# Kernel optimization log

Hardware: AMD Instinct MI355X
Metric: run time of the kernel (lower is better)

Reference implementation:

```python
import jax, jax.numpy as jnp
import numpy as np

EPS = 1e-12  # matches torch.nn.functional.normalize eps

def _l2norm(x, axis=-1):
    n = jnp.sqrt(jnp.sum(x * x, axis=axis, keepdims=True))
    return x / jnp.maximum(n, EPS)

def setup_inputs() -> dict:
    key = jax.random.key(0)
    k1, k2 = jax.random.split(key)
    B, C, H, W = 16, 256, 32, 32
    K = 8192
    z = jax.random.normal(k1, (B, C, H, W), dtype=jnp.float32)
    # torch init: uniform(-1/K, 1/K)
    emb_weight = jax.random.uniform(k2, (K, C), dtype=jnp.float32,
                                    minval=-1.0 / K, maxval=1.0 / K)
    return {"z": z, "emb_weight": emb_weight}

def reference(z, emb_weight):
    B, C, H, W = z.shape
    zt = jnp.transpose(z, (0, 2, 3, 1))            # [B,H,W,C]
    z_flat = zt.reshape(-1, C)                      # [N,C]
    zf_n = _l2norm(z_flat)                          # normalized tokens
    e_n = _l2norm(emb_weight)                       # normalized codebook [K,C]
    # squared euclidean distance via matmul (N x K)
    d = (jnp.sum(zf_n * zf_n, axis=1, keepdims=True)
         + jnp.sum(e_n * e_n, axis=1)
         - 2.0 * jnp.einsum('nc,kc->nk', zf_n, e_n))
    idx = jnp.argmin(d, axis=1)                     # [N]
    # get_codebook_entry: gather raw weight then normalize
    zq = _l2norm(emb_weight[idx])                   # [N,C]
    zq = zq.reshape(B, H, W, C)
    z_n = _l2norm(zt)                               # normalize z over channel dim
    # straight-through estimator
    zq = z_n + jax.lax.stop_gradient(zq - z_n)
    out = jnp.transpose(zq, (0, 3, 1, 2))           # [B,C,H,W]
    indices = idx.reshape(B, H, W)
    return out, indices
```

## Files before the change

### kernel.cpp

```cpp
#include <hip/hip_runtime.h>
#include <math.h>
#include <float.h>

#define K_CODES 8192
#define C_DIM   256
#define N_TOK   16384
#define B_      16
#define H_      32
#define W_      32
#define HW      1024
#define KSPLIT  16
#define TOKS_PER_BLK 256

typedef short  short8   __attribute__((ext_vector_type(8)));
typedef float  floatx16 __attribute__((ext_vector_type(16)));

__device__ inline ushort f32_to_bf16_rne(float x) {
    union { float f; unsigned u; } v; v.f = x;
    unsigned u = v.u;
    return (ushort)((u + 0x7FFFu + ((u >> 16) & 1u)) >> 16);
}
__device__ inline float bf16_bits_to_f32(ushort h) {
    union { unsigned u; float f; } v; v.u = ((unsigned)h) << 16;
    return v.f;
}
__device__ inline unsigned umax_(unsigned a, unsigned b) { return a > b ? a : b; }
__device__ inline unsigned umin_(unsigned a, unsigned b) { return a < b ? a : b; }

__device__ inline void g2l16(const void* g, void* l) {
    __builtin_amdgcn_global_load_lds((const __attribute__((address_space(1))) unsigned int*)g,
                                     (__attribute__((address_space(3))) unsigned int*)l,
                                     16, 0, 0);
}


__global__ __launch_bounds__(256) void norm_pack(
        const float* __restrict__ emb, const float* __restrict__ z,
        float* __restrict__ e_n, float* __restrict__ s2,
        ushort* __restrict__ Chi,
        float* __restrict__ ztn, ushort* __restrict__ Thi) {
    __shared__ float tile[32][257];
    __shared__ float pvt[32][9];
    __shared__ float pvt2[32][9];
    __shared__ float inv[32];
    int t = threadIdx.x;
    int bid = blockIdx.x;
    if (bid < 256) {
        int k0 = bid * 32;
        int r = t >> 3, cp = t & 7;
        const float* src = emb + (size_t)(k0 + r) * C_DIM + cp * 32;
        float ss = 0.f;
        #pragma unroll
        for (int j = 0; j < 8; ++j) {
            float4 v = *(const float4*)(src + j * 4);
            tile[r][cp * 32 + j * 4 + 0] = v.x;
            tile[r][cp * 32 + j * 4 + 1] = v.y;
            tile[r][cp * 32 + j * 4 + 2] = v.z;
            tile[r][cp * 32 + j * 4 + 3] = v.w;
            ss = fmaf(v.x, v.x, ss); ss = fmaf(v.y, v.y, ss);
            ss = fmaf(v.z, v.z, ss); ss = fmaf(v.w, v.w, ss);
        }
        pvt[r][cp] = ss;
        __syncthreads();
        if (t < 32) {
            float a = 0.f;
            #pragma unroll
            for (int p = 0; p < 8; ++p) a += pvt[t][p];
            inv[t] = 1.0f / fmaxf(sqrtf(a), 1e-12f);
        }
        __syncthreads();
        float iv = inv[r];
        float s2p = 0.f;
        float* dst = e_n + (size_t)(k0 + r) * C_DIM + cp * 32;
        #pragma unroll
        for (int j = 0; j < 8; ++j) {
            float a = tile[r][cp * 32 + j * 4 + 0] * iv;
            float b = tile[r][cp * 32 + j * 4 + 1] * iv;
            float c = tile[r][cp * 32 + j * 4 + 2] * iv;
            float d = tile[r][cp * 32 + j * 4 + 3] * iv;
            s2p = fmaf(a, a, s2p); s2p = fmaf(b, b, s2p);
            s2p = fmaf(c, c, s2p); s2p = fmaf(d, d, s2p);
            float4 o = {a, b, c, d};
            *(float4*)(dst + j * 4) = o;
        }
        pvt2[r][cp] = s2p;
        __syncthreads();
        if (t < 32) {
            float a = 0.f;
            #pragma unroll
            for (int p = 0; p < 8; ++p) a += pvt2[t][p];
            s2[k0 + t] = a;
        }
        char* chiB = (char*)Chi;
        #pragma unroll
        for (int e = 0; e < 4; ++e) {
            int p = e * 256 + t;
            int row = p & 31;
            int ch0 = ((p >> 6) << 4) | (((p >> 5) & 1) << 3);
            float rv = inv[row];
            union { ushort u[8]; uint4 v; } hs;
            #pragma unroll
            for (int i = 0; i < 8; ++i)
                hs.u[i] = f32_to_bf16_rne(tile[row][ch0 + i] * rv);
            size_t addr = (size_t)bid * 16384 + (size_t)p * 16;
            *(uint4*)(chiB + addr) = hs.v;
        }
    } else {
        int tb = bid - 256;
        int b = tb >> 5, h = tb & 31;
        int w = t & 31, c0 = t >> 5;
        const float* zb = z + ((size_t)(b * C_DIM) * H_ + h) * W_;
        #pragma unroll
        for (int it = 0; it < 32; ++it) {
            int c = it * 8 + c0;
            tile[w][c] = zb[(size_t)c * HW + w];
        }
        __syncthreads();
        int part = t >> 5, w2 = t & 31;
        float s = 0.f;
        #pragma unroll
        for (int i = 0; i < 32; ++i) {
            float v = tile[w2][part * 32 + i];
            s = fmaf(v, v, s);
        }
        pvt[w2][part] = s;
        __syncthreads();
        if (t < 32) {
            float ss = 0.f;
            #pragma unroll
            for (int p = 0; p < 8; ++p) ss += pvt[t][p];
            inv[t] = 1.0f / fmaxf(sqrtf(ss), 1e-12f);
        }
        __syncthreads();
        int n_base = tb * 32;
        for (int r = 0; r < 32; ++r) {
            float val = tile[r][t] * inv[r];
            ztn[(size_t)(n_base + r) * C_DIM + t] = val;
        }
        char* thiB = (char*)Thi;
        #pragma unroll
        for (int e = 0; e < 4; ++e) {
            int p = e * 256 + t;
            int row = p & 31;
            int ch0 = ((p >> 6) << 4) | (((p >> 5) & 1) << 3);
            float rv = inv[row];
            union { ushort u[8]; uint4 v; } hs;
            #pragma unroll
            for (int i = 0; i < 8; ++i)
                hs.u[i] = f32_to_bf16_rne(tile[row][ch0 + i] * rv);
            size_t addr = (size_t)tb * 16384 + (size_t)p * 16;
            *(uint4*)(thiB + addr) = hs.v;
        }
    }
}

__global__ __launch_bounds__(256, 2) void score_topk(
        const ushort* __restrict__ Chi,
        const ushort* __restrict__ Thi, uint2* __restrict__ cand) {
    __shared__ __align__(16) char smem[24576];
    int t = threadIdx.x;
    int l = t & 63, wv = t >> 6;
    int hh = l >> 5, col = l & 31;
    int tokBase = blockIdx.x * TOKS_PER_BLK;
    int tokRG = tokBase >> 5;
    int part = blockIdx.y;
    int partBase = part * (K_CODES / KSPLIT);
    int codeRGbase = partBase >> 5;

    const char* chiB = (const char*)Chi;
    const char* thiB = (const char*)Thi;

    unsigned rv1[2] = {0u, 0u}, rv2[2] = {0u, 0u}, rv3[2] = {0u, 0u};
    int ri1[2] = {0, 0}, ri2[2] = {0, 0}, ri3[2] = {0, 0};

    auto stage = [&](int skt, int ss, char* buf) {
        int codeRG = codeRGbase + skt * 4;
        #pragma unroll
        for (int gi = 0; gi < 3; ++gi) {
            int slice = wv * 3 + gi;
            const char* gb;
            int off;
            if (slice < 4) {
                gb = chiB + (size_t)(codeRG + slice) * 16384;
                off = slice << 10;
            } else {
                int trg = slice - 4;
                gb = thiB + (size_t)(tokRG + trg) * 16384;
                off = 4096 + (trg << 10);
            }
            g2l16(gb + ss * 1024 + (l << 4), buf + off);
        }
    };

    stage(0, 0, smem);

    for (int kt = 0; kt < 4; ++kt) {
        floatx16 acc[4][2];
        #pragma unroll
        for (int ct = 0; ct < 4; ++ct)
            #pragma unroll
            for (int nt = 0; nt < 2; ++nt)
                #pragma unroll
                for (int r = 0; r < 16; ++r) acc[ct][nt][r] = 0.f;

        for (int s = 0; s < 16; ++s) {
            int gidx = kt * 16 + s;
            __syncthreads();
            int nidx = gidx + 1;
            if (nidx < 64)
                stage(nidx >> 4, nidx & 15, smem + ((nidx & 1) ? 12288 : 0));
            const char* buf = smem + ((gidx & 1) ? 12288 : 0);

            short8 bh[2];
            #pragma unroll
            for (int nt = 0; nt < 2; ++nt) {
                int trg = wv * 2 + nt;
                bh[nt] = *(const short8*)(buf + 4096 + (trg << 10) + (l << 4));
            }
            #pragma unroll
            for (int ct = 0; ct < 4; ++ct) {
                short8 ah = *(const short8*)(buf + (ct << 10) + (l << 4));
                #pragma unroll
                for (int nt = 0; nt < 2; ++nt) {
                    acc[ct][nt] = __builtin_amdgcn_mfma_f32_32x32x16_bf16(ah, bh[nt], acc[ct][nt], 0, 0, 0);
                }
            }
        }

        int kbase = partBase + kt * 128;
        #pragma unroll
        for (int nt = 0; nt < 2; ++nt) {
            unsigned m1 = 0u, m2 = 0u, m3 = 0u;
            #pragma unroll
            for (int ct = 0; ct < 4; ++ct) {
                #pragma unroll
                for (int r = 0; r < 16; ++r) {
                    unsigned key = (__float_as_uint(fmaf(acc[ct][nt][r], 0.25f, 1.25f)) & 0xFFFFFFC0u)
                                   | (unsigned)((ct << 4) | r);
                    unsigned t1 = umin_(m1, key); m1 = umax_(m1, key);
                    unsigned t2 = umin_(m2, t1);  m2 = umax_(m2, t1);
                    m3 = umax_(m3, t2);
                }
            }
            unsigned mm[3] = {m1, m2, m3};
            #pragma unroll
            for (int j = 0; j < 3; ++j) {
                unsigned k = mm[j];
                int o = (int)(k & 63u), r = o & 15;
                int c = kbase + ((o >> 4) << 5) + (r & 3) + 8 * (r >> 2) + 4 * hh;
                if (k > rv1[nt]) {
                    rv3[nt] = rv2[nt]; ri3[nt] = ri2[nt];
                    rv2[nt] = rv1[nt]; ri2[nt] = ri1[nt];
                    rv1[nt] = k; ri1[nt] = c;
                } else if (k > rv2[nt]) {
                    rv3[nt] = rv2[nt]; ri3[nt] = ri2[nt];
                    rv2[nt] = k; ri2[nt] = c;
                } else if (k > rv3[nt]) {
                    rv3[nt] = k; ri3[nt] = c;
                }
            }
        }
    }

    __syncthreads();
    unsigned* mk = (unsigned*)smem;
    int*      mi = (int*)(smem + 8192);
    #pragma unroll
    for (int nt = 0; nt < 2; ++nt) {
        int base = (wv * 64 + nt * 32 + col) * 6 + hh * 3;
        mk[base + 0] = rv1[nt]; mi[base + 0] = ri1[nt];
        mk[base + 1] = rv2[nt]; mi[base + 1] = ri2[nt];
        mk[base + 2] = rv3[nt]; mi[base + 2] = ri3[nt];
    }
    __syncthreads();
    {
        unsigned b1 = 0u, b2 = 0u, b3 = 0u;
        int i1 = 0x7FFFFFFF, i2 = 0x7FFFFFFF, i3 = 0x7FFFFFFF;
        #pragma unroll
        for (int j = 0; j < 6; ++j) {
            unsigned k = mk[t * 6 + j]; int i = mi[t * 6 + j];
            if (k > b1 || (k == b1 && i < i1)) {
                b3 = b2; i3 = i2; b2 = b1; i2 = i1; b1 = k; i1 = i;
            } else if (k > b2 || (k == b2 && i < i2)) {
                b3 = b2; i3 = i2; b2 = k; i2 = i;
            } else if (k > b3 || (k == b3 && i < i3)) {
                b3 = k; i3 = i;
            }
        }
        size_t base = ((size_t)part * N_TOK + tokBase + t) * 3;
        cand[base + 0] = {b1, (unsigned)i1};
        cand[base + 1] = {b2, (unsigned)i2};
        cand[base + 2] = {b3, (unsigned)i3};
    }
}

__global__ __launch_bounds__(256) void rescore_gather(
        const float* __restrict__ ztn, const float* __restrict__ e_n,
        const float* __restrict__ s2, const uint2* __restrict__ cand,
        float* __restrict__ out, float* __restrict__ idxf) {
    __shared__ __align__(16) char sm[32 * 257 * 4];
    __shared__ uint2 cd[32][48];
    __shared__ int idxs[32];
    __shared__ int slowlist[32];
    __shared__ int nslow;
    float* tile = (float*)sm;
    int t = threadIdx.x;
    int bid = blockIdx.x;
    int b = bid >> 5, h = bid & 31;
    int n_base = bid * 32;
    int wv = t >> 6, l = t & 63;

    if (t == 0) nslow = 0;
    {
        int tok = t >> 3, p = t & 7;
        int n = n_base + tok;
        #pragma unroll
        for (int slot = 0; slot < 3; ++slot) {
            cd[tok][p * 3 + slot]        = cand[((size_t)p * N_TOK + n) * 3 + slot];
            cd[tok][(p + 8) * 3 + slot]  = cand[((size_t)(p + 8) * N_TOK + n) * 3 + slot];
        }
    }
    __syncthreads();

    if (t < 32) {
        unsigned b1k = 0u, b2k = 0u; int b1i = 0x7FFFFFFF, b2i = 0x7FFFFFFF;
        #pragma unroll
        for (int p = 0; p < 48; ++p) {
            uint2 c2 = cd[t][p];
            unsigned k = c2.x; int i = (int)c2.y;
            if (k > b1k || (k == b1k && i < b1i)) { b2k = b1k; b2i = b1i; b1k = k; b1i = i; }
            else if (k > b2k || (k == b2k && i < b2i)) { b2k = k; b2i = i; }
        }
        if (b1k - b2k > 2048u) {
            idxs[t] = b1i;
            idxf[n_base + t] = (float)b1i;
        } else {
            int s = atomicAdd(&nslow, 1);
            slowlist[s] = t;
        }
    }
    __syncthreads();
    int ns = nslow;
    for (int j = wv; j < ns; j += 4) {
        int tok = slowlist[j];
        int n = n_base + tok;
        float bs = FLT_MAX; int bi = 0x7FFFFFFF;
        if (l < 48) {
            int c = (int)cd[tok][l].y;
            const float* er = e_n + (size_t)c * C_DIM;
            const float* zr = ztn + (size_t)n * C_DIM;
            float s = 0.f;
            #pragma unroll
            for (int jj = 0; jj < 64; ++jj) {
                float4 e4 = *(const float4*)(er + jj * 4);
                float4 z4 = *(const float4*)(zr + jj * 4);
                s = fmaf(e4.x, z4.x, s); s = fmaf(e4.y, z4.y, s);
                s = fmaf(e4.z, z4.z, s); s = fmaf(e4.w, z4.w, s);
            }
            bs = s2[c] - 2.f * s;
            bi = c;
        }
        #pragma unroll
        for (int d = 1; d < 64; d <<= 1) {
            float os = __shfl_xor(bs, d);
            int   oi = __shfl_xor(bi, d);
            if (os < bs || (os == bs && oi < bi)) { bs = os; bi = oi; }
        }
        if (l == 0) { idxs[tok] = bi; idxf[n] = (float)bi; }
    }
    __syncthreads();

    for (int r = 0; r < 32; ++r) {
        int k = idxs[r];
        tile[r * 257 + t] = e_n[(size_t)k * C_DIM + t];
    }
    __syncthreads();
    int w = t & 31, c0 = t >> 5;
    float* ob = out + ((size_t)(b * C_DIM) * H_ + h) * W_;
    #pragma unroll
    for (int it = 0; it < 32; ++it) {
        int c = it * 8 + c0;
        ob[(size_t)c * HW + w] = tile[w * 257 + c];
    }
}

extern "C" void kernel_launch(void* const* d_in, const int* in_sizes, int n_in,
                              void* d_out, int out_size, void* d_ws, size_t ws_size,
                              hipStream_t stream) {
    const float* z   = (const float*)d_in[0];
    const float* emb = (const float*)d_in[1];
    float* out  = (float*)d_out;
    float* idxf = out + (size_t)B_ * C_DIM * H_ * W_;

    char* ws = (char*)d_ws;
    size_t o = 0;
    float*  e_n  = (float*)(ws + o);  o += (size_t)K_CODES * C_DIM * 4;
    float*  s2   = (float*)(ws + o);  o += 32768;
    float*  ztn  = (float*)(ws + o);  o += (size_t)N_TOK * C_DIM * 4;
    ushort* Chi  = (ushort*)(ws + o); o += (size_t)K_CODES * C_DIM * 2;
    ushort* Thi  = (ushort*)(ws + o); o += (size_t)N_TOK * C_DIM * 2;
    uint2*  cand = (uint2*)(ws + o);  o += (size_t)KSPLIT * N_TOK * 3 * 8;

    hipLaunchKernelGGL(norm_pack, dim3(256 + B_ * H_), dim3(256), 0, stream,
                       emb, z, e_n, s2, Chi, ztn, Thi);
    hipLaunchKernelGGL(score_topk, dim3(N_TOK / TOKS_PER_BLK, KSPLIT), dim3(256), 0, stream,
                       Chi, Thi, cand);
    hipLaunchKernelGGL(rescore_gather, dim3(B_ * H_), dim3(256), 0, stream,
                       ztn, e_n, s2, cand, out, idxf);
}
```

Baseline: 184.3 us.

## Keep token fragments in registers and stage full code k-tiles per barrier

Each wave now loads its 32-token bf16 fragments for the whole channel dimension into registers once, so token data no longer goes through shared memory. Codebook tiles are staged as whole 64-code by 256-channel blocks, double-buffered in 64 KB of LDS. That cuts barriers from one per 16-channel slice to one per 64-code tile. The per-tile accumulator set is halved to 2x2, so the top-k key pack uses 5 bits of the 6-bit index field and the code-index mapping must stay consistent. The trade-off is higher register pressure from 32 short8 values plus larger LDS, which may hurt occupancy at two blocks per CU.

```diff
diff --git a/kernel.cpp b/kernel.cpp
--- a/kernel.cpp
+++ b/kernel.cpp
@@ -157,7 +157,7 @@
 __global__ __launch_bounds__(256, 2) void score_topk(
         const ushort* __restrict__ Chi,
         const ushort* __restrict__ Thi, uint2* __restrict__ cand) {
-    __shared__ __align__(16) char smem[24576];
+    __shared__ __align__(16) char smem[65536];
     int t = threadIdx.x;
     int l = t & 63, wv = t >> 6;
     int hh = l >> 5, col = l & 31;
@@ -170,69 +170,61 @@
     const char* chiB = (const char*)Chi;
     const char* thiB = (const char*)Thi;
 
+    short8 tok[2][16];
+    #pragma unroll
+    for (int nt = 0; nt < 2; ++nt) {
+        const char* tb = thiB + (size_t)(tokRG + wv * 2 + nt) * 16384 + (l << 4);
+        #pragma unroll
+        for (int s = 0; s < 16; ++s)
+            tok[nt][s] = *(const short8*)(tb + s * 1024);
+    }
+
+    auto stage = [&](int kt) {
+        char* buf = smem + ((kt & 1) << 15);
+        int codeRG = codeRGbase + kt * 2;
+        #pragma unroll
+        for (int gi = 0; gi < 8; ++gi) {
+            int sl = wv * 8 + gi;
+            const char* gb = chiB + (size_t)(codeRG + (sl >> 4)) * 16384
+                           + ((sl & 15) << 10) + (l << 4);
+            g2l16(gb, buf + (sl << 10));
+        }
+    };
+
+    stage(0);
+
     unsigned rv1[2] = {0u, 0u}, rv2[2] = {0u, 0u}, rv3[2] = {0u, 0u};
     int ri1[2] = {0, 0}, ri2[2] = {0, 0}, ri3[2] = {0, 0};
 
-    auto stage = [&](int skt, int ss, char* buf) {
-        int codeRG = codeRGbase + skt * 4;
-        #pragma unroll
-        for (int gi = 0; gi < 3; ++gi) {
-            int slice = wv * 3 + gi;
-            const char* gb;
-            int off;
-            if (slice < 4) {
-                gb = chiB + (size_t)(codeRG + slice) * 16384;
-                off = slice << 10;
-            } else {
-                int trg = slice - 4;
-                gb = thiB + (size_t)(tokRG + trg) * 16384;
-                off = 4096 + (trg << 10);
-            }
-            g2l16(gb + ss * 1024 + (l << 4), buf + off);
-        }
-    };
-
-    stage(0, 0, smem);
-
-    for (int kt = 0; kt < 4; ++kt) {
-        floatx16 acc[4][2];
-        #pragma unroll
-        for (int ct = 0; ct < 4; ++ct)
+    for (int kt = 0; kt < 8; ++kt) {
+        __syncthreads();
+        if (kt < 7) stage(kt + 1);
+        const char* buf = smem + ((kt & 1) << 15);
+
+        floatx16 acc[2][2];
+        #pragma unroll
+        for (int ct = 0; ct < 2; ++ct)
             #pragma unroll
             for (int nt = 0; nt < 2; ++nt)
                 #pragma unroll
                 for (int r = 0; r < 16; ++r) acc[ct][nt][r] = 0.f;
 
+        #pragma unroll
         for (int s = 0; s < 16; ++s) {
-            int gidx = kt * 16 + s;
-            __syncthreads();
-            int nidx = gidx + 1;
-            if (nidx < 64)
-                stage(nidx >> 4, nidx & 15, smem + ((nidx & 1) ? 12288 : 0));
-            const char* buf = smem + ((gidx & 1) ? 12288 : 0);
-
-            short8 bh[2];
-            #pragma unroll
-            for (int nt = 0; nt < 2; ++nt) {
-                int trg = wv * 2 + nt;
-                bh[nt] = *(const short8*)(buf + 4096 + (trg << 10) + (l << 4));
-            }
-            #pragma unroll
-            for (int ct = 0; ct < 4; ++ct) {
-                short8 ah = *(const short8*)(buf + (ct << 10) + (l << 4));
-                #pragma unroll
-                for (int nt = 0; nt < 2; ++nt) {
-                    acc[ct][nt] = __builtin_amdgcn_mfma_f32_32x32x16_bf16(ah, bh[nt], acc[ct][nt], 0, 0, 0);
-                }
-            }
-        }
-
-        int kbase = partBase + kt * 128;
+            short8 a0 = *(const short8*)(buf + (s << 10) + (l << 4));
+            short8 a1 = *(const short8*)(buf + 16384 + (s << 10) + (l << 4));
+            acc[0][0] = __builtin_amdgcn_mfma_f32_32x32x16_bf16(a0, tok[0][s], acc[0][0], 0, 0, 0);
+            acc[0][1] = __builtin_amdgcn_mfma_f32_32x32x16_bf16(a0, tok[1][s], acc[0][1], 0, 0, 0);
+            acc[1][0] = __builtin_amdgcn_mfma_f32_32x32x16_bf16(a1, tok[0][s], acc[1][0], 0, 0, 0);
+            acc[1][1] = __builtin_amdgcn_mfma_f32_32x32x16_bf16(a1, tok[1][s], acc[1][1], 0, 0, 0);
+        }
+
+        int kbase = partBase + kt * 64;
         #pragma unroll
         for (int nt = 0; nt < 2; ++nt) {
             unsigned m1 = 0u, m2 = 0u, m3 = 0u;
             #pragma unroll
-            for (int ct = 0; ct < 4; ++ct) {
+            for (int ct = 0; ct < 2; ++ct) {
                 #pragma unroll
                 for (int r = 0; r < 16; ++r) {
                     unsigned key = (__float_as_uint(fmaf(acc[ct][nt][r], 0.25f, 1.25f)) & 0xFFFFFFC0u)
```

New measurement: 193.9 us. 1.05x slower.
